# Kernel optimization log

Measured on AMD Instinct MI355X. Metric: run time of the kernel, lower is better.

## Reference

```python
import jax, jax.numpy as jnp
import numpy as np
from jax import lax

# 8-bit symmetric quantization: clip bound = 2**(prec-1) - 1
CLIP = 127.0
EPS = 1e-6  # epsilon in scale denominator to avoid div-by-zero (mirrors QuantOps bound epsilon)


def setup_inputs() -> dict:
    key = jax.random.key(0)
    k1, k2 = jax.random.split(key)
    B, CIN, COUT = 8192, 4096, 8192
    act = jax.random.normal(k1, (B, CIN), dtype=jnp.float32)
    w = jax.random.normal(k2, (CIN, COUT), dtype=jnp.float32)
    return {"act": act, "w": w}


def reference(act, w):
    # --- activation quantization: per-input-channel symmetric scale, shape (1, Cin) ---
    act_bound = jnp.max(jnp.abs(act), axis=0, keepdims=True) + EPS     # (1, Cin)
    act_scale = CLIP / act_bound                                        # (1, Cin)
    act_q = jnp.clip(jnp.round(act * act_scale), -CLIP, CLIP)           # int values in fp32

    # fold inverse activation scale into weight rows: w_scaled_rows = (1/act_scale) * w
    w_scaled = w * (1.0 / act_scale).reshape(-1, 1)                     # (Cin, Cout)

    # --- weight quantization: per-output-channel symmetric scale, shape (1, Cout) ---
    w_bound = jnp.max(jnp.abs(w_scaled), axis=0, keepdims=True) + EPS   # (1, Cout)
    w_scale = CLIP / w_bound                                            # (1, Cout)
    w_q = jnp.clip(jnp.round(w_scaled * w_scale), -CLIP, CLIP)

    out_i32 = lax.dot_general(
        act_q.astype(jnp.int8),
        w_q.astype(jnp.int8),
        dimension_numbers=(((1,), (0,)), ((), ())),
        preferred_element_type=jnp.int32,
    )
    out = out_i32.astype(jnp.float32)

    # inline dequant by per-output-channel weight scale (act scale already folded into w)
    return (out * (1.0 / w_scale)).astype(jnp.float32)
```

## Files before the change

### kernel.cpp

```cpp
#include <hip/hip_runtime.h>
#include <hip/hip_bf16.h>
#include <stdint.h>

#define BDIM 8192
#define CIN  4096
#define COUT 8192
#define EPSQ 1e-6f

typedef int v4i __attribute__((ext_vector_type(4)));

#define GLD16_TO_LDS(gp, lp)                                                   \
    __builtin_amdgcn_global_load_lds(                                          \
        (const __attribute__((address_space(1))) void*)(gp),                   \
        (__attribute__((address_space(3))) void*)(lp), 16, 0, 0)

__device__ __forceinline__ int q8i(float x) {
    float r = rintf(x);
    r = fminf(127.0f, fmaxf(-127.0f, r));
    return (int)r;
}

__global__ void act_absmax_kernel(const float* __restrict__ act,
                                  int* __restrict__ amax_bits) {
    int c4 = (blockIdx.x << 8) + threadIdx.x;
    int r0 = blockIdx.y << 7;
    const float4* p = (const float4*)act + (size_t)r0 * (CIN / 4) + c4;
    float mx = 0.f, my = 0.f, mz = 0.f, mw = 0.f;
#pragma unroll 4
    for (int r = 0; r < 128; ++r) {
        float4 v = p[(size_t)r * (CIN / 4)];
        mx = fmaxf(mx, fabsf(v.x));
        my = fmaxf(my, fabsf(v.y));
        mz = fmaxf(mz, fabsf(v.z));
        mw = fmaxf(mw, fabsf(v.w));
    }
    int c = c4 << 2;
    atomicMax(amax_bits + c + 0, __float_as_int(mx));
    atomicMax(amax_bits + c + 1, __float_as_int(my));
    atomicMax(amax_bits + c + 2, __float_as_int(mz));
    atomicMax(amax_bits + c + 3, __float_as_int(mw));
}

__global__ void act_quant_kernel(const float4* __restrict__ act4,
                                 const int4* __restrict__ amax_bits4,
                                 float* __restrict__ inv_as,
                                 int* __restrict__ actq_packed) {
    int flat4 = blockIdx.x * 256 + threadIdx.x;
    int c4 = flat4 & ((CIN / 4) - 1);
    float4 v = act4[flat4];
    int4 mb = amax_bits4[c4];
    float sx = 127.0f / (__int_as_float(mb.x) + EPSQ);
    float sy = 127.0f / (__int_as_float(mb.y) + EPSQ);
    float sz = 127.0f / (__int_as_float(mb.z) + EPSQ);
    float sw = 127.0f / (__int_as_float(mb.w) + EPSQ);
    int q0 = q8i(v.x * sx), q1 = q8i(v.y * sy), q2 = q8i(v.z * sz), q3 = q8i(v.w * sw);
    int packed = (q0 & 0xff) | ((q1 & 0xff) << 8) | ((q2 & 0xff) << 16) | ((q3 & 0xff) << 24);
    actq_packed[flat4] = packed;
    if (flat4 < CIN / 4) {
        int c = c4 << 2;
        inv_as[c + 0] = 1.0f / sx;
        inv_as[c + 1] = 1.0f / sy;
        inv_as[c + 2] = 1.0f / sz;
        inv_as[c + 3] = 1.0f / sw;
    }
}

__global__ void w_absmax_kernel(const float* __restrict__ w,
                                const float* __restrict__ inv_as,
                                int* __restrict__ wmax_bits) {
    int c4 = (blockIdx.x << 8) + threadIdx.x;
    int k0 = blockIdx.y << 6;
    const float4* p = (const float4*)w + (size_t)k0 * (COUT / 4) + c4;
    float mx = 0.f, my = 0.f, mz = 0.f, mw = 0.f;
#pragma unroll 4
    for (int r = 0; r < 64; ++r) {
        float ia = inv_as[k0 + r];
        float4 v = p[(size_t)r * (COUT / 4)];
        mx = fmaxf(mx, fabsf(v.x * ia));
        my = fmaxf(my, fabsf(v.y * ia));
        mz = fmaxf(mz, fabsf(v.z * ia));
        mw = fmaxf(mw, fabsf(v.w * ia));
    }
    int c = c4 << 2;
    atomicMax(wmax_bits + c + 0, __float_as_int(mx));
    atomicMax(wmax_bits + c + 1, __float_as_int(my));
    atomicMax(wmax_bits + c + 2, __float_as_int(mz));
    atomicMax(wmax_bits + c + 3, __float_as_int(mw));
}

__global__ void w_quant_t_kernel(const float* __restrict__ w,
                                 const float* __restrict__ inv_as,
                                 const int* __restrict__ wmax_bits,
                                 signed char* __restrict__ wqT) {
    __shared__ int tile32[16][65];
    int t = threadIdx.x;
    int k0 = blockIdx.x << 6;
    int j0 = blockIdx.y << 6;
    int tx = t & 63;
    int ty = t >> 6;
    int j = j0 + tx;
    float wscale = 127.0f / (__int_as_float(wmax_bits[j]) + EPSQ);
#pragma unroll
    for (int r = 0; r < 4; ++r) {
        int a = r * 4 + ty;
        int kb = k0 + (a << 2);
        int packed = 0;
#pragma unroll
        for (int u = 0; u < 4; ++u) {
            int k = kb + u;
            float wsc = w[(size_t)k * COUT + j] * inv_as[k];
            int q = q8i(wsc * wscale);
            packed |= (q & 0xff) << (8 * u);
        }
        tile32[a][tx] = packed;
    }
    __syncthreads();
    int j_loc = t >> 2;
    int c = t & 3;
    int4 v;
    v.x = tile32[c * 4 + 0][j_loc];
    v.y = tile32[c * 4 + 1][j_loc];
    v.z = tile32[c * 4 + 2][j_loc];
    v.w = tile32[c * 4 + 3][j_loc];
    *(int4*)(wqT + (size_t)(j0 + j_loc) * CIN + k0 + c * 16) = v;
}

__global__ __launch_bounds__(256) void gemm_i8_kernel(
    const signed char* __restrict__ Aq,
    const signed char* __restrict__ Bq,
    const int* __restrict__ wmax_bits,
    float* __restrict__ out) {
    __shared__ __align__(16) signed char As[128 * 64];
    __shared__ __align__(16) signed char Bs[128 * 64];

    const int tid = threadIdx.x;
    const int wave = tid >> 6;
    const int lane = tid & 63;
    const int bm = blockIdx.y << 7;
    const int bn = blockIdx.x << 7;
    const int wm = (wave >> 1) << 6;
    const int wn = (wave & 1) << 6;

    const int g = lane >> 4;
    const int l16 = lane & 15;

    v4i acc[4][4] = {};

    for (int kt = 0; kt < CIN; kt += 64) {
        __syncthreads();
#pragma unroll
        for (int t = 0; t < 2; ++t) {
            int c0 = (wave * 2 + t) * 64;
            int mm = (t << 6) + lane;
            int gg = wave;
            const signed char* ga = Aq + ((size_t)(bm + mm) << 12) + kt + (gg << 4);
            GLD16_TO_LDS(ga, As + (c0 << 4));
            const signed char* gb = Bq + ((size_t)(bn + mm) << 12) + kt + (gg << 4);
            GLD16_TO_LDS(gb, Bs + (c0 << 4));
        }
        __syncthreads();

        v4i af[4], bf[4];
#pragma unroll
        for (int t = 0; t < 4; ++t)
            af[t] = *(const v4i*)(As + (((g << 7) + wm + (t << 4) + l16) << 4));
#pragma unroll
        for (int t = 0; t < 4; ++t)
            bf[t] = *(const v4i*)(Bs + (((g << 7) + wn + (t << 4) + l16) << 4));

#pragma unroll
        for (int tm = 0; tm < 4; ++tm)
#pragma unroll
            for (int tn = 0; tn < 4; ++tn)
                acc[tm][tn] = __builtin_amdgcn_mfma_i32_16x16x64_i8(
                    af[tm], bf[tn], acc[tm][tn], 0, 0, 0);
    }

#pragma unroll
    for (int tn = 0; tn < 4; ++tn) {
        int col = bn + wn + (tn << 4) + l16;
        float wscale = 127.0f / (__int_as_float(wmax_bits[col]) + EPSQ);
        float invws = 1.0f / wscale;
#pragma unroll
        for (int tm = 0; tm < 4; ++tm) {
            int row0 = bm + wm + (tm << 4) + (g << 2);
#pragma unroll
            for (int r = 0; r < 4; ++r)
                out[((size_t)(row0 + r) << 13) + col] = (float)acc[tm][tn][r] * invws;
        }
    }
}

extern "C" void kernel_launch(void* const* d_in, const int* in_sizes, int n_in,
                              void* d_out, int out_size, void* d_ws, size_t ws_size,
                              hipStream_t stream) {
    const float* act = (const float*)d_in[0];
    const float* w   = (const float*)d_in[1];
    float* out = (float*)d_out;
    char* ws = (char*)d_ws;

    int*   amax_bits = (int*)ws;
    float* inv_as    = (float*)(ws + 16384);
    int*   wmax_bits = (int*)(ws + 32768);
    signed char* actq = (signed char*)(ws + 65536);
    signed char* wqT  = (signed char*)(ws + 65536 + (size_t)BDIM * CIN);

    act_absmax_kernel<<<dim3(4, 64), 256, 0, stream>>>(act, amax_bits);
    act_quant_kernel<<<(BDIM * CIN / 4) / 256, 256, 0, stream>>>(
        (const float4*)act, (const int4*)amax_bits, inv_as, (int*)actq);
    w_absmax_kernel<<<dim3(8, 64), 256, 0, stream>>>(w, inv_as, wmax_bits);
    w_quant_t_kernel<<<dim3(64, 128), 256, 0, stream>>>(w, inv_as, wmax_bits, wqT);
    gemm_i8_kernel<<<dim3(COUT / 128, BDIM / 128), 256, 0, stream>>>(
        actq, wqT, wmax_bits, out);
}
```

Baseline: 987.0 us.

## Switch GEMM to 32x32x32 int8 MFMA with 128-deep K tiles; widen absmax grids

The int8 GEMM now uses the 32x32x32 MFMA instruction with a 2x2 accumulator grid per wave, where it previously used a 4x4 grid of 16x16x64 MFMAs. The K tile per LDS stage grows from 64 to 128, and the load, fragment and store indexing are rewritten to match. This is meant to halve the number of barriers per K and cut LDS fragment reads per MFMA. The absmax reduction kernels also get more blocks with fewer rows each, to improve occupancy at the cost of more atomics. LDS use doubles to 32KB per block, which may reduce occupancy.

```diff
diff --git a/kernel.cpp b/kernel.cpp
--- a/kernel.cpp
+++ b/kernel.cpp
@@ -7,7 +7,8 @@
 #define COUT 8192
 #define EPSQ 1e-6f
 
-typedef int v4i __attribute__((ext_vector_type(4)));
+typedef int v4i  __attribute__((ext_vector_type(4)));
+typedef int v16i __attribute__((ext_vector_type(16)));
 
 #define GLD16_TO_LDS(gp, lp)                                                   \
     __builtin_amdgcn_global_load_lds(                                          \
@@ -23,11 +24,11 @@
 __global__ void act_absmax_kernel(const float* __restrict__ act,
                                   int* __restrict__ amax_bits) {
     int c4 = (blockIdx.x << 8) + threadIdx.x;
-    int r0 = blockIdx.y << 7;
+    int r0 = blockIdx.y << 5;
     const float4* p = (const float4*)act + (size_t)r0 * (CIN / 4) + c4;
     float mx = 0.f, my = 0.f, mz = 0.f, mw = 0.f;
 #pragma unroll 4
-    for (int r = 0; r < 128; ++r) {
+    for (int r = 0; r < 32; ++r) {
         float4 v = p[(size_t)r * (CIN / 4)];
         mx = fmaxf(mx, fabsf(v.x));
         my = fmaxf(my, fabsf(v.y));
@@ -69,11 +70,11 @@
                                 const float* __restrict__ inv_as,
                                 int* __restrict__ wmax_bits) {
     int c4 = (blockIdx.x << 8) + threadIdx.x;
-    int k0 = blockIdx.y << 6;
+    int k0 = blockIdx.y << 5;
     const float4* p = (const float4*)w + (size_t)k0 * (COUT / 4) + c4;
     float mx = 0.f, my = 0.f, mz = 0.f, mw = 0.f;
 #pragma unroll 4
-    for (int r = 0; r < 64; ++r) {
+    for (int r = 0; r < 32; ++r) {
         float ia = inv_as[k0 + r];
         float4 v = p[(size_t)r * (COUT / 4)];
         mx = fmaxf(mx, fabsf(v.x * ia));
@@ -130,8 +131,8 @@
     const signed char* __restrict__ Bq,
     const int* __restrict__ wmax_bits,
     float* __restrict__ out) {
-    __shared__ __align__(16) signed char As[128 * 64];
-    __shared__ __align__(16) signed char Bs[128 * 64];
+    __shared__ __align__(16) signed char As[128 * 128];
+    __shared__ __align__(16) signed char Bs[128 * 128];
 
     const int tid = threadIdx.x;
     const int wave = tid >> 6;
@@ -141,52 +142,57 @@
     const int wm = (wave >> 1) << 6;
     const int wn = (wave & 1) << 6;
 
-    const int g = lane >> 4;
-    const int l16 = lane & 15;
-
-    v4i acc[4][4] = {};
-
-    for (int kt = 0; kt < CIN; kt += 64) {
+    const int l32 = lane & 31;
+    const int kh2 = lane >> 5;
+
+    v16i acc[2][2] = {};
+
+    for (int kt = 0; kt < CIN; kt += 128) {
         __syncthreads();
 #pragma unroll
-        for (int t = 0; t < 2; ++t) {
-            int c0 = (wave * 2 + t) * 64;
-            int mm = (t << 6) + lane;
-            int gg = wave;
-            const signed char* ga = Aq + ((size_t)(bm + mm) << 12) + kt + (gg << 4);
+        for (int t = 0; t < 4; ++t) {
+            int idx = (wave << 2) + t;
+            int kh = idx >> 1;
+            int m0 = (idx & 1) << 6;
+            int c0 = (kh << 7) + m0;
+            const signed char* ga = Aq + ((size_t)(bm + m0 + lane) << 12) + kt + (kh << 4);
             GLD16_TO_LDS(ga, As + (c0 << 4));
-            const signed char* gb = Bq + ((size_t)(bn + mm) << 12) + kt + (gg << 4);
+            const signed char* gb = Bq + ((size_t)(bn + m0 + lane) << 12) + kt + (kh << 4);
             GLD16_TO_LDS(gb, Bs + (c0 << 4));
         }
         __syncthreads();
 
-        v4i af[4], bf[4];
-#pragma unroll
-        for (int t = 0; t < 4; ++t)
-            af[t] = *(const v4i*)(As + (((g << 7) + wm + (t << 4) + l16) << 4));
-#pragma unroll
-        for (int t = 0; t < 4; ++t)
-            bf[t] = *(const v4i*)(Bs + (((g << 7) + wn + (t << 4) + l16) << 4));
-
-#pragma unroll
-        for (int tm = 0; tm < 4; ++tm)
-#pragma unroll
-            for (int tn = 0; tn < 4; ++tn)
-                acc[tm][tn] = __builtin_amdgcn_mfma_i32_16x16x64_i8(
-                    af[tm], bf[tn], acc[tm][tn], 0, 0, 0);
-    }
-
-#pragma unroll
-    for (int tn = 0; tn < 4; ++tn) {
-        int col = bn + wn + (tn << 4) + l16;
+#pragma unroll
+        for (int s = 0; s < 4; ++s) {
+            int kh = (s << 1) + kh2;
+            v4i af[2], bf[2];
+#pragma unroll
+            for (int u = 0; u < 2; ++u) {
+                af[u] = *(const v4i*)(As + (((kh << 7) + wm + (u << 5) + l32) << 4));
+                bf[u] = *(const v4i*)(Bs + (((kh << 7) + wn + (u << 5) + l32) << 4));
+            }
+#pragma unroll
+            for (int um = 0; um < 2; ++um)
+#pragma unroll
+                for (int un = 0; un < 2; ++un)
+                    acc[um][un] = __builtin_amdgcn_mfma_i32_32x32x32_i8(
+                        af[um], bf[un], acc[um][un], 0, 0, 0);
+        }
+    }
+
+#pragma unroll
+    for (int un = 0; un < 2; ++un) {
+        int col = bn + wn + (un << 5) + l32;
         float wscale = 127.0f / (__int_as_float(wmax_bits[col]) + EPSQ);
         float invws = 1.0f / wscale;
 #pragma unroll
-        for (int tm = 0; tm < 4; ++tm) {
-            int row0 = bm + wm + (tm << 4) + (g << 2);
-#pragma unroll
-            for (int r = 0; r < 4; ++r)
-                out[((size_t)(row0 + r) << 13) + col] = (float)acc[tm][tn][r] * invws;
+        for (int um = 0; um < 2; ++um) {
+            int rb = bm + wm + (um << 5) + (kh2 << 2);
+#pragma unroll
+            for (int reg = 0; reg < 16; ++reg) {
+                int row = rb + (reg & 3) + ((reg >> 2) << 3);
+                out[((size_t)row << 13) + col] = (float)acc[um][un][reg] * invws;
+            }
         }
     }
 }
@@ -205,10 +211,10 @@
     signed char* actq = (signed char*)(ws + 65536);
     signed char* wqT  = (signed char*)(ws + 65536 + (size_t)BDIM * CIN);
 
-    act_absmax_kernel<<<dim3(4, 64), 256, 0, stream>>>(act, amax_bits);
+    act_absmax_kernel<<<dim3(4, 256), 256, 0, stream>>>(act, amax_bits);
     act_quant_kernel<<<(BDIM * CIN / 4) / 256, 256, 0, stream>>>(
         (const float4*)act, (const int4*)amax_bits, inv_as, (int*)actq);
-    w_absmax_kernel<<<dim3(8, 64), 256, 0, stream>>>(w, inv_as, wmax_bits);
+    w_absmax_kernel<<<dim3(8, 128), 256, 0, stream>>>(w, inv_as, wmax_bits);
     w_quant_t_kernel<<<dim3(64, 128), 256, 0, stream>>>(w, inv_as, wmax_bits, wqT);
     gemm_i8_kernel<<<dim3(COUT / 128, BDIM / 128), 256, 0, stream>>>(
         actq, wqT, wmax_bits, out);
```

Result: slower. 1.070 ms (+8.4%).
